# Optimization experiments

Hardware: AMD Instinct MI355X
Metric: run time of the kernel (lower is better)

The kernel has to match this reference:

```python
import jax, jax.numpy as jnp
import numpy as np

N_NODES = 40000
N_EDGES = 640000


def _sage_conv(x, src, dst, W_nb, b, W_self, n_nodes):
    # message = x[src] gathered per edge; mean-aggregate at dst (PyG SAGEConv, aggr='mean')
    msgs = x[src]  # [E, d]
    agg = jax.ops.segment_sum(msgs, dst, num_segments=n_nodes)  # [N, d]
    deg = jax.ops.segment_sum(jnp.ones((src.shape[0],), dtype=x.dtype), dst, num_segments=n_nodes)
    mean = agg / jnp.maximum(deg, 1.0)[:, None]
    # lin_l(aggregated) with bias + lin_r(self) without bias
    return mean @ W_nb + b + x @ W_self


def setup_inputs() -> dict:
    key = jax.random.key(0)
    ks = jax.random.split(key, 8)
    in_dim, h1, h2, out_dim = 128, 128, 64, 40
    s = lambda k, shp, d: jax.random.normal(k, shp, dtype=jnp.float32) / np.sqrt(d)
    return {
        "x": jax.random.normal(ks[0], (N_NODES, in_dim), dtype=jnp.float32),
        "edge_index": jax.random.randint(ks[1], (2, N_EDGES), 0, N_NODES, dtype=jnp.int64) if jax.config.jax_enable_x64 else jax.random.randint(ks[1], (2, N_EDGES), 0, N_NODES).astype(jnp.int32),
        "W1_nb": s(ks[2], (in_dim, h1), in_dim),
        "b1": jnp.zeros((h1,), dtype=jnp.float32),
        "W1_self": s(ks[3], (in_dim, h1), in_dim),
        "W2_nb": s(ks[4], (h1, h2), h1),
        "b2": jnp.zeros((h2,), dtype=jnp.float32),
        "W2_self": s(ks[5], (h1, h2), h1),
        "Wfc": s(ks[6], (h2, out_dim), h2),
        "bfc": jnp.zeros((out_dim,), dtype=jnp.float32),
    }


def reference(x, edge_index, W1_nb, b1, W1_self, W2_nb, b2, W2_self, Wfc, bfc):
    src, dst = edge_index[0], edge_index[1]
    h = jax.nn.relu(_sage_conv(x, src, dst, W1_nb, b1, W1_self, N_NODES))
    h = jax.nn.relu(_sage_conv(h, src, dst, W2_nb, b2, W2_self, N_NODES))
    embedding = h
    logits = h @ Wfc + bfc
    return (embedding, logits)
```

## Files before the change

### kernel.cpp

```cpp
#include <hip/hip_runtime.h>
#include <hip/hip_bf16.h>


#define N_NODES 40000
#define N_EDGES 640000
#define D_IN    128
#define D_H1    128
#define D_H2    64
#define D_OUT   40

#define SCAN_BLK 1024
#define N_SCAN_BLKS ((N_NODES + SCAN_BLK - 1) / SCAN_BLK)

typedef __attribute__((ext_vector_type(8))) short short8v;
typedef __attribute__((ext_vector_type(4))) float float4v;

__device__ __forceinline__ unsigned short f2bf(float f) {
    unsigned u = __float_as_uint(f);
    unsigned r = u + 0x7FFFu + ((u >> 16) & 1u);
    return (unsigned short)(r >> 16);
}
__device__ __forceinline__ float bf2f(unsigned short b) {
    return __uint_as_float(((unsigned)b) << 16);
}


__global__ void hist_k(const int* __restrict__ dst, int* __restrict__ deg) {
    int e = blockIdx.x * blockDim.x + threadIdx.x;
    if (e < N_EDGES) atomicAdd(&deg[dst[e]], 1);
}

__global__ __launch_bounds__(SCAN_BLK) void scan1_k(const int* __restrict__ deg,
                                                    int* __restrict__ blocksum) {
    __shared__ int wsum[SCAN_BLK / 64];
    int t = threadIdx.x;
    int i = blockIdx.x * SCAN_BLK + t;
    int v = (i < N_NODES) ? deg[i] : 0;
    #pragma unroll
    for (int s = 32; s > 0; s >>= 1) v += __shfl_down(v, s);
    if ((t & 63) == 0) wsum[t >> 6] = v;
    __syncthreads();
    if (t < SCAN_BLK / 64) {
        int x = wsum[t];
        #pragma unroll
        for (int s = SCAN_BLK / 128; s > 0; s >>= 1) x += __shfl_down(x, s);
        if (t == 0) blocksum[blockIdx.x] = x;
    }
}

__global__ __launch_bounds__(SCAN_BLK) void scan3_k(const int* __restrict__ deg,
                                                    const int* __restrict__ blocksum,
                                                    int* __restrict__ offsets,
                                                    int* __restrict__ cursor) {
    __shared__ int sm[SCAN_BLK];
    __shared__ int base_s;
    int t = threadIdx.x;
    int i = blockIdx.x * SCAN_BLK + t;
    if (t == 0) {
        int b = 0;
        for (int j = 0; j < (int)blockIdx.x; j++) b += blocksum[j];
        base_s = b;
        if (blockIdx.x == N_SCAN_BLKS - 1)
            offsets[N_NODES] = b + blocksum[blockIdx.x];
    }
    int v = (i < N_NODES) ? deg[i] : 0;
    sm[t] = v;
    __syncthreads();
    for (int s = 1; s < SCAN_BLK; s <<= 1) {
        int u = (t >= s) ? sm[t - s] : 0;
        __syncthreads();
        sm[t] += u;
        __syncthreads();
    }
    if (i < N_NODES) {
        int excl = base_s + sm[t] - v;
        offsets[i] = excl;
        cursor[i] = excl;
    }
}

__global__ void place_k(const int* __restrict__ src, const int* __restrict__ dst,
                        int* __restrict__ cursor, int* __restrict__ src_sorted) {
    int e = blockIdx.x * blockDim.x + threadIdx.x;
    if (e < N_EDGES) {
        int p = atomicAdd(&cursor[dst[e]], 1);
        src_sorted[p] = src[e];
    }
}


template <int D, int STRIDE>
__global__ __launch_bounds__(256) void agg_k(const float* __restrict__ feat,
                                             const int* __restrict__ offsets,
                                             const int* __restrict__ srcs,
                                             float* __restrict__ mean_out) {
    constexpr int LPN = D / 4;
    constexpr int NPB = 256 / LPN;
    int t = threadIdx.x;
    int g = t / LPN;
    int q = t % LPN;
    int node = blockIdx.x * NPB + g;
    int beg = offsets[node];
    int end = offsets[node + 1];
    float4 accA = {0.f, 0.f, 0.f, 0.f}, accB = {0.f, 0.f, 0.f, 0.f};
    int i = beg;
    for (; i + 8 <= end; i += 8) {
        float4 v[8];
        #pragma unroll
        for (int j = 0; j < 8; j++) {
            int s = srcs[i + j];
            v[j] = *(const float4*)(feat + (size_t)s * STRIDE + q * 4);
        }
        #pragma unroll
        for (int j = 0; j < 4; j++) {
            accA.x += v[j].x; accA.y += v[j].y; accA.z += v[j].z; accA.w += v[j].w;
            accB.x += v[j+4].x; accB.y += v[j+4].y; accB.z += v[j+4].z; accB.w += v[j+4].w;
        }
    }
    for (; i < end; ++i) {
        float4 v = *(const float4*)(feat + (size_t)srcs[i] * STRIDE + q * 4);
        accA.x += v.x; accA.y += v.y; accA.z += v.z; accA.w += v.w;
    }
    int cnt = end - beg;
    float inv = 1.0f / (float)(cnt > 1 ? cnt : 1);
    float4 r;
    r.x = (accA.x + accB.x) * inv; r.y = (accA.y + accB.y) * inv;
    r.z = (accA.z + accB.z) * inv; r.w = (accA.w + accB.w) * inv;
    *(float4*)(mean_out + (size_t)node * D + q * 4) = r;
}


__device__ __forceinline__ void wsplit_one(const float* W, int K, int N, int tid,
                                           short* Wt_hi, short* Wt_lo) {
    int k = tid / N, n = tid - k * N;
    float w = W[tid];
    unsigned short h = f2bf(w);
    unsigned short lo = f2bf(w - bf2f(h));
    Wt_hi[n * K + k] = (short)h;
    Wt_lo[n * K + k] = (short)lo;
}

__global__ void wsplit_all_k(const float* __restrict__ W1nb, const float* __restrict__ W1sf,
                             const float* __restrict__ W2nb, const float* __restrict__ W2sf,
                             short* __restrict__ o1nbh, short* __restrict__ o1nbl,
                             short* __restrict__ o1sfh, short* __restrict__ o1sfl,
                             short* __restrict__ o2nbh, short* __restrict__ o2nbl,
                             short* __restrict__ o2sfh, short* __restrict__ o2sfl) {
    int tid = blockIdx.x * blockDim.x + threadIdx.x;
    if (tid < 16384)      wsplit_one(W1nb, 128, 128, tid,          o1nbh, o1nbl);
    else if (tid < 32768) wsplit_one(W1sf, 128, 128, tid - 16384,  o1sfh, o1sfl);
    else if (tid < 40960) wsplit_one(W2nb, 128, 64,  tid - 32768,  o2nbh, o2nbl);
    else if (tid < 49152) wsplit_one(W2sf, 128, 64,  tid - 40960,  o2sfh, o2sfl);
}


template <int NOUT>
__global__ __launch_bounds__(256) void sage_mfma_k(
    const float* __restrict__ A1, const float* __restrict__ A2,
    const short* __restrict__ W1h, const short* __restrict__ W1l,
    const short* __restrict__ W2h, const short* __restrict__ W2l,
    const float* __restrict__ bias, float* __restrict__ out) {
    __shared__ short wh_s[64 * 128];
    __shared__ short wl_s[64 * 128];

    const int t = threadIdx.x;
    const int w = t >> 6;
    const int l = t & 63;
    const int ln16 = l & 15;
    const int kgrp = l >> 4;
    const int arow = blockIdx.x * 32 + (w & 1) * 16 + ln16;
    const int colbase = blockIdx.y * 64;
    const int cw = (w >> 1) * 32;

    float4v acc[2];
    #pragma unroll
    for (int ct = 0; ct < 2; ct++) {
        float bv = bias[colbase + cw + ct * 16 + ln16];
        acc[ct] = (float4v){bv, bv, bv, bv};
    }

    for (int phase = 0; phase < 2; ++phase) {
        const float* __restrict__ A  = phase ? A2 : A1;
        const short* __restrict__ Wh = phase ? W2h : W1h;
        const short* __restrict__ Wl = phase ? W2l : W1l;

        __syncthreads();

        float4 a0[4], a1[4];
        const float* ap = A + (size_t)arow * 128 + kgrp * 8;
        #pragma unroll
        for (int kc = 0; kc < 4; kc++) {
            a0[kc] = *(const float4*)(ap + kc * 32);
            a1[kc] = *(const float4*)(ap + kc * 32 + 4);
        }

        #pragma unroll
        for (int it = 0; it < 4; it++) {
            int fid = t + it * 256;
            int r = fid >> 4, c = fid & 15;
            int gofs = (colbase + r) * 128 + c * 8;
            int byte = (r * 256 + c * 16) ^ ((r & 7) << 4);
            *(int4*)((char*)wh_s + byte) = *(const int4*)(Wh + gofs);
            *(int4*)((char*)wl_s + byte) = *(const int4*)(Wl + gofs);
        }

        short8v ah[4], al[4];
        #pragma unroll
        for (int kc = 0; kc < 4; kc++) {
            #pragma unroll
            for (int j = 0; j < 4; j++) {
                float f0 = (&a0[kc].x)[j];
                float f1 = (&a1[kc].x)[j];
                unsigned short h0 = f2bf(f0), h1 = f2bf(f1);
                ah[kc][j]     = (short)h0;
                ah[kc][j + 4] = (short)h1;
                al[kc][j]     = (short)f2bf(f0 - bf2f(h0));
                al[kc][j + 4] = (short)f2bf(f1 - bf2f(h1));
            }
        }

        __syncthreads();

        #pragma unroll
        for (int kc = 0; kc < 4; kc++) {
            #pragma unroll
            for (int ct = 0; ct < 2; ct++) {
                int col = cw + ct * 16 + ln16;
                int byte = (col * 256 + kc * 64 + kgrp * 16) ^ ((col & 7) << 4);
                short8v bh = *(const short8v*)((const char*)wh_s + byte);
                short8v bl = *(const short8v*)((const char*)wl_s + byte);
                acc[ct] = __builtin_amdgcn_mfma_f32_16x16x32_bf16(ah[kc], bh, acc[ct], 0, 0, 0);
                acc[ct] = __builtin_amdgcn_mfma_f32_16x16x32_bf16(ah[kc], bl, acc[ct], 0, 0, 0);
                acc[ct] = __builtin_amdgcn_mfma_f32_16x16x32_bf16(al[kc], bh, acc[ct], 0, 0, 0);
            }
        }
    }

    #pragma unroll
    for (int ct = 0; ct < 2; ct++) {
        #pragma unroll
        for (int r = 0; r < 4; r++) {
            int row = blockIdx.x * 32 + (w & 1) * 16 + kgrp * 4 + r;
            int col = colbase + cw + ct * 16 + ln16;
            out[(size_t)row * NOUT + col] = fmaxf(acc[ct][r], 0.f);
        }
    }
}


__global__ __launch_bounds__(256) void gemm2_k(
    const float* __restrict__ A,
    const short* __restrict__ Wnbh, const short* __restrict__ Wnbl,
    const short* __restrict__ Wsfh, const short* __restrict__ Wsfl,
    const float* __restrict__ b2, float* __restrict__ zs2) {
    __shared__ short wh_s[64 * 128];
    __shared__ short wl_s[64 * 128];

    const int t = threadIdx.x;
    const int w = t >> 6;
    const int l = t & 63;
    const int ln16 = l & 15;
    const int kgrp = l >> 4;
    const int arow = blockIdx.x * 32 + (w & 1) * 16 + ln16;
    const int ysel = blockIdx.y;
    const int cw = (w >> 1) * 32;

    const short* __restrict__ Wh = ysel ? Wsfh : Wnbh;
    const short* __restrict__ Wl = ysel ? Wsfl : Wnbl;

    float4v acc[2];
    #pragma unroll
    for (int ct = 0; ct < 2; ct++) {
        float bv = ysel ? b2[cw + ct * 16 + ln16] : 0.f;
        acc[ct] = (float4v){bv, bv, bv, bv};
    }

    float4 a0[4], a1[4];
    const float* ap = A + (size_t)arow * 128 + kgrp * 8;
    #pragma unroll
    for (int kc = 0; kc < 4; kc++) {
        a0[kc] = *(const float4*)(ap + kc * 32);
        a1[kc] = *(const float4*)(ap + kc * 32 + 4);
    }

    #pragma unroll
    for (int it = 0; it < 4; it++) {
        int fid = t + it * 256;
        int r = fid >> 4, c = fid & 15;
        int gofs = r * 128 + c * 8;
        int byte = (r * 256 + c * 16) ^ ((r & 7) << 4);
        *(int4*)((char*)wh_s + byte) = *(const int4*)(Wh + gofs);
        *(int4*)((char*)wl_s + byte) = *(const int4*)(Wl + gofs);
    }

    short8v ah[4], al[4];
    #pragma unroll
    for (int kc = 0; kc < 4; kc++) {
        #pragma unroll
        for (int j = 0; j < 4; j++) {
            float f0 = (&a0[kc].x)[j];
            float f1 = (&a1[kc].x)[j];
            unsigned short h0 = f2bf(f0), h1 = f2bf(f1);
            ah[kc][j]     = (short)h0;
            ah[kc][j + 4] = (short)h1;
            al[kc][j]     = (short)f2bf(f0 - bf2f(h0));
            al[kc][j + 4] = (short)f2bf(f1 - bf2f(h1));
        }
    }

    __syncthreads();

    #pragma unroll
    for (int kc = 0; kc < 4; kc++) {
        #pragma unroll
        for (int ct = 0; ct < 2; ct++) {
            int col = cw + ct * 16 + ln16;
            int byte = (col * 256 + kc * 64 + kgrp * 16) ^ ((col & 7) << 4);
            short8v bh = *(const short8v*)((const char*)wh_s + byte);
            short8v bl = *(const short8v*)((const char*)wl_s + byte);
            acc[ct] = __builtin_amdgcn_mfma_f32_16x16x32_bf16(ah[kc], bh, acc[ct], 0, 0, 0);
            acc[ct] = __builtin_amdgcn_mfma_f32_16x16x32_bf16(ah[kc], bl, acc[ct], 0, 0, 0);
            acc[ct] = __builtin_amdgcn_mfma_f32_16x16x32_bf16(al[kc], bh, acc[ct], 0, 0, 0);
        }
    }

    #pragma unroll
    for (int ct = 0; ct < 2; ct++) {
        #pragma unroll
        for (int r = 0; r < 4; r++) {
            int row = blockIdx.x * 32 + (w & 1) * 16 + kgrp * 4 + r;
            int col = ysel * 64 + cw + ct * 16 + ln16;
            zs2[(size_t)row * 128 + col] = acc[ct][r];
        }
    }
}


__global__ __launch_bounds__(256) void final_k(const float* __restrict__ mean2,
                                               const float* __restrict__ zs2,
                                               const float* __restrict__ Wfc,
                                               const float* __restrict__ bfc,
                                               float* __restrict__ emb,
                                               float* __restrict__ logits) {
    __shared__ float es[16][68];
    int t = threadIdx.x;
    int g = t >> 4;
    int q = t & 15;
    int node = blockIdx.x * 16 + g;
    float4 m = *(const float4*)(mean2 + (size_t)node * 64 + q * 4);
    float4 s = *(const float4*)(zs2 + (size_t)node * 128 + 64 + q * 4);
    float4 e;
    e.x = fmaxf(m.x + s.x, 0.f);
    e.y = fmaxf(m.y + s.y, 0.f);
    e.z = fmaxf(m.z + s.z, 0.f);
    e.w = fmaxf(m.w + s.w, 0.f);
    *(float4*)(emb + (size_t)node * 64 + q * 4) = e;
    *(float4*)&es[g][q * 4] = e;
    __syncthreads();
    #pragma unroll
    for (int j = 0; j < 3; j++) {
        int c = q + 16 * j;
        if (c < D_OUT) {
            float acc = bfc[c];
            #pragma unroll
            for (int k = 0; k < 64; k++) acc += es[g][k] * Wfc[k * D_OUT + c];
            logits[(size_t)node * D_OUT + c] = acc;
        }
    }
}


extern "C" void kernel_launch(void* const* d_in, const int* in_sizes, int n_in,
                              void* d_out, int out_size, void* d_ws, size_t ws_size,
                              hipStream_t stream) {
    const float* x       = (const float*)d_in[0];
    const int*   ei      = (const int*)d_in[1];
    const float* W1_nb   = (const float*)d_in[2];
    const float* b1      = (const float*)d_in[3];
    const float* W1_self = (const float*)d_in[4];
    const float* W2_nb   = (const float*)d_in[5];
    const float* b2      = (const float*)d_in[6];
    const float* W2_self = (const float*)d_in[7];
    const float* Wfc     = (const float*)d_in[8];
    const float* bfc     = (const float*)d_in[9];

    const int* src = ei;
    const int* dst = ei + N_EDGES;

    char* w = (char*)d_ws;
    int* deg        = (int*)w;
    int* offsets    = deg + N_NODES;
    int* cursor     = offsets + (N_NODES + 1);
    int* blocksum   = cursor + N_NODES;
    int* src_sorted = blocksum + N_SCAN_BLKS;
    size_t int_elems = (size_t)N_NODES * 3 + 1 + N_SCAN_BLKS + N_EDGES;
    size_t int_bytes = (int_elems * 4 + 15) & ~(size_t)15;
    float* bufA = (float*)(w + int_bytes);
    float* bufB = bufA + (size_t)N_NODES * 128;
    short* w1nb_h   = (short*)(bufB + (size_t)N_NODES * 128);
    short* w1nb_l   = w1nb_h + 128 * 128;
    short* w1self_h = w1nb_l + 128 * 128;
    short* w1self_l = w1self_h + 128 * 128;
    short* w2nb_h   = w1self_l + 128 * 128;
    short* w2nb_l   = w2nb_h + 128 * 64;
    short* w2self_h = w2nb_l + 128 * 64;
    short* w2self_l = w2self_h + 128 * 64;

    float* emb    = (float*)d_out;
    float* logits = emb + (size_t)N_NODES * D_H2;

    wsplit_all_k<<<(49152 + 255) / 256, 256, 0, stream>>>(
        W1_nb, W1_self, W2_nb, W2_self,
        w1nb_h, w1nb_l, w1self_h, w1self_l, w2nb_h, w2nb_l, w2self_h, w2self_l);

    hipMemsetAsync(deg, 0, N_NODES * sizeof(int), stream);
    hist_k<<<(N_EDGES + 255) / 256, 256, 0, stream>>>(dst, deg);
    scan1_k<<<N_SCAN_BLKS, SCAN_BLK, 0, stream>>>(deg, blocksum);
    scan3_k<<<N_SCAN_BLKS, SCAN_BLK, 0, stream>>>(deg, blocksum, offsets, cursor);
    place_k<<<(N_EDGES + 255) / 256, 256, 0, stream>>>(src, dst, cursor, src_sorted);

    agg_k<128, 128><<<N_NODES / 8, 256, 0, stream>>>(x, offsets, src_sorted, bufA);
    sage_mfma_k<128><<<dim3(N_NODES / 32, 2), 256, 0, stream>>>(
        bufA, x, w1nb_h, w1nb_l, w1self_h, w1self_l, b1, bufB);

    gemm2_k<<<dim3(N_NODES / 32, 2), 256, 0, stream>>>(
        bufB, w2nb_h, w2nb_l, w2self_h, w2self_l, b2, bufA);

    agg_k<64, 128><<<N_NODES / 16, 256, 0, stream>>>(bufA, offsets, src_sorted, bufB);

    final_k<<<N_NODES / 16, 256, 0, stream>>>(bufB, bufA, Wfc, bfc, emb, logits);
}
```

Before: 294.0 us.

## Gather neighbor features in fp16 and fuse layer-2 aggregation with final projection

Converts x to fp16 up front so the layer-1 neighbor gather moves half the bytes per edge. The layer-2 neighbor projection is also written as fp16 into a compact 64-wide buffer. The second aggregation is fused with the bias/ReLU/logits kernel, which removes one launch and one intermediate round trip. Storing the gathered features in fp16 adds rounding error compared with the fp32 gathers and may loosen accuracy. An extra conversion pass over x is added.

After: 264.1 us. 1.11x faster.

```diff
diff --git a/kernel.cpp b/kernel.cpp
--- a/kernel.cpp
+++ b/kernel.cpp
@@ -1,5 +1,6 @@
 #include <hip/hip_runtime.h>
 #include <hip/hip_bf16.h>
+#include <hip/hip_fp16.h>
 
 
 #define N_NODES 40000
@@ -13,6 +14,7 @@
 #define N_SCAN_BLKS ((N_NODES + SCAN_BLK - 1) / SCAN_BLK)
 
 typedef __attribute__((ext_vector_type(8))) short short8v;
+typedef __attribute__((ext_vector_type(8))) _Float16 half8v;
 typedef __attribute__((ext_vector_type(4))) float float4v;
 
 __device__ __forceinline__ unsigned short f2bf(float f) {
@@ -89,12 +91,24 @@
 }
 
 
-template <int D, int STRIDE>
-__global__ __launch_bounds__(256) void agg_k(const float* __restrict__ feat,
-                                             const int* __restrict__ offsets,
-                                             const int* __restrict__ srcs,
-                                             float* __restrict__ mean_out) {
-    constexpr int LPN = D / 4;
+__global__ void xh_k(const float* __restrict__ x, _Float16* __restrict__ xh) {
+    int i = blockIdx.x * blockDim.x + threadIdx.x;
+    if (i >= N_NODES * D_IN / 8) return;
+    float4 a = ((const float4*)x)[i * 2];
+    float4 b = ((const float4*)x)[i * 2 + 1];
+    half8v h;
+    h[0] = (_Float16)a.x; h[1] = (_Float16)a.y; h[2] = (_Float16)a.z; h[3] = (_Float16)a.w;
+    h[4] = (_Float16)b.x; h[5] = (_Float16)b.y; h[6] = (_Float16)b.z; h[7] = (_Float16)b.w;
+    ((half8v*)xh)[i] = h;
+}
+
+
+template <int D>
+__global__ __launch_bounds__(256) void aggh_k(const _Float16* __restrict__ feat,
+                                              const int* __restrict__ offsets,
+                                              const int* __restrict__ srcs,
+                                              float* __restrict__ mean_out) {
+    constexpr int LPN = D / 8;
     constexpr int NPB = 256 / LPN;
     int t = threadIdx.x;
     int g = t / LPN;
@@ -102,31 +116,31 @@
     int node = blockIdx.x * NPB + g;
     int beg = offsets[node];
     int end = offsets[node + 1];
-    float4 accA = {0.f, 0.f, 0.f, 0.f}, accB = {0.f, 0.f, 0.f, 0.f};
+    float acc[8] = {0.f, 0.f, 0.f, 0.f, 0.f, 0.f, 0.f, 0.f};
     int i = beg;
     for (; i + 8 <= end; i += 8) {
-        float4 v[8];
+        half8v v[8];
+        #pragma unroll
+        for (int j = 0; j < 8; j++)
+            v[j] = *(const half8v*)(feat + (size_t)srcs[i + j] * D + q * 8);
         #pragma unroll
         for (int j = 0; j < 8; j++) {
-            int s = srcs[i + j];
-            v[j] = *(const float4*)(feat + (size_t)s * STRIDE + q * 4);
-        }
-        #pragma unroll
-        for (int j = 0; j < 4; j++) {
-            accA.x += v[j].x; accA.y += v[j].y; accA.z += v[j].z; accA.w += v[j].w;
-            accB.x += v[j+4].x; accB.y += v[j+4].y; accB.z += v[j+4].z; accB.w += v[j+4].w;
+            #pragma unroll
+            for (int k = 0; k < 8; k++) acc[k] += (float)v[j][k];
         }
     }
     for (; i < end; ++i) {
-        float4 v = *(const float4*)(feat + (size_t)srcs[i] * STRIDE + q * 4);
-        accA.x += v.x; accA.y += v.y; accA.z += v.z; accA.w += v.w;
+        half8v v = *(const half8v*)(feat + (size_t)srcs[i] * D + q * 8);
+        #pragma unroll
+        for (int k = 0; k < 8; k++) acc[k] += (float)v[k];
     }
     int cnt = end - beg;
     float inv = 1.0f / (float)(cnt > 1 ? cnt : 1);
-    float4 r;
-    r.x = (accA.x + accB.x) * inv; r.y = (accA.y + accB.y) * inv;
-    r.z = (accA.z + accB.z) * inv; r.w = (accA.w + accB.w) * inv;
-    *(float4*)(mean_out + (size_t)node * D + q * 4) = r;
+    float4 r0, r1;
+    r0.x = acc[0] * inv; r0.y = acc[1] * inv; r0.z = acc[2] * inv; r0.w = acc[3] * inv;
+    r1.x = acc[4] * inv; r1.y = acc[5] * inv; r1.z = acc[6] * inv; r1.w = acc[7] * inv;
+    *(float4*)(mean_out + (size_t)node * D + q * 8) = r0;
+    *(float4*)(mean_out + (size_t)node * D + q * 8 + 4) = r1;
 }
 
 
@@ -252,7 +266,8 @@
     const float* __restrict__ A,
     const short* __restrict__ Wnbh, const short* __restrict__ Wnbl,
     const short* __restrict__ Wsfh, const short* __restrict__ Wsfl,
-    const float* __restrict__ b2, float* __restrict__ zs2) {
+    const float* __restrict__ b2,
+    _Float16* __restrict__ z2nb, float* __restrict__ zself) {
     __shared__ short wh_s[64 * 128];
     __shared__ short wl_s[64 * 128];
 
@@ -329,43 +344,77 @@
         #pragma unroll
         for (int r = 0; r < 4; r++) {
             int row = blockIdx.x * 32 + (w & 1) * 16 + kgrp * 4 + r;
-            int col = ysel * 64 + cw + ct * 16 + ln16;
-            zs2[(size_t)row * 128 + col] = acc[ct][r];
-        }
-    }
-}
-
-
-__global__ __launch_bounds__(256) void final_k(const float* __restrict__ mean2,
-                                               const float* __restrict__ zs2,
-                                               const float* __restrict__ Wfc,
-                                               const float* __restrict__ bfc,
-                                               float* __restrict__ emb,
-                                               float* __restrict__ logits) {
-    __shared__ float es[16][68];
+            int col = cw + ct * 16 + ln16;
+            if (ysel == 0) z2nb[(size_t)row * 64 + col] = (_Float16)acc[ct][r];
+            else           zself[(size_t)row * 64 + col] = acc[ct][r];
+        }
+    }
+}
+
+
+__global__ __launch_bounds__(256) void agg2final_k(const _Float16* __restrict__ z2nb,
+                                                   const float* __restrict__ zself,
+                                                   const int* __restrict__ offsets,
+                                                   const int* __restrict__ srcs,
+                                                   const float* __restrict__ Wfc,
+                                                   const float* __restrict__ bfc,
+                                                   float* __restrict__ emb,
+                                                   float* __restrict__ logits) {
+    __shared__ float es[32][68];
     int t = threadIdx.x;
-    int g = t >> 4;
-    int q = t & 15;
-    int node = blockIdx.x * 16 + g;
-    float4 m = *(const float4*)(mean2 + (size_t)node * 64 + q * 4);
-    float4 s = *(const float4*)(zs2 + (size_t)node * 128 + 64 + q * 4);
-    float4 e;
-    e.x = fmaxf(m.x + s.x, 0.f);
-    e.y = fmaxf(m.y + s.y, 0.f);
-    e.z = fmaxf(m.z + s.z, 0.f);
-    e.w = fmaxf(m.w + s.w, 0.f);
-    *(float4*)(emb + (size_t)node * 64 + q * 4) = e;
-    *(float4*)&es[g][q * 4] = e;
+    int g = t >> 3;
+    int q = t & 7;
+    int node = blockIdx.x * 32 + g;
+    int beg = offsets[node];
+    int end = offsets[node + 1];
+    float acc[8] = {0.f, 0.f, 0.f, 0.f, 0.f, 0.f, 0.f, 0.f};
+    int i = beg;
+    for (; i + 8 <= end; i += 8) {
+        half8v v[8];
+        #pragma unroll
+        for (int j = 0; j < 8; j++)
+            v[j] = *(const half8v*)(z2nb + (size_t)srcs[i + j] * 64 + q * 8);
+        #pragma unroll
+        for (int j = 0; j < 8; j++) {
+            #pragma unroll
+            for (int k = 0; k < 8; k++) acc[k] += (float)v[j][k];
+        }
+    }
+    for (; i < end; ++i) {
+        half8v v = *(const half8v*)(z2nb + (size_t)srcs[i] * 64 + q * 8);
+        #pragma unroll
+        for (int k = 0; k < 8; k++) acc[k] += (float)v[k];
+    }
+    int cnt = end - beg;
+    float inv = 1.0f / (float)(cnt > 1 ? cnt : 1);
+    float4 s0 = *(const float4*)(zself + (size_t)node * 64 + q * 8);
+    float4 s1 = *(const float4*)(zself + (size_t)node * 64 + q * 8 + 4);
+    float e[8];
+    e[0] = fmaxf(acc[0] * inv + s0.x, 0.f);
+    e[1] = fmaxf(acc[1] * inv + s0.y, 0.f);
+    e[2] = fmaxf(acc[2] * inv + s0.z, 0.f);
+    e[3] = fmaxf(acc[3] * inv + s0.w, 0.f);
+    e[4] = fmaxf(acc[4] * inv + s1.x, 0.f);
+    e[5] = fmaxf(acc[5] * inv + s1.y, 0.f);
+    e[6] = fmaxf(acc[6] * inv + s1.z, 0.f);
+    e[7] = fmaxf(acc[7] * inv + s1.w, 0.f);
+    float4 o0 = {e[0], e[1], e[2], e[3]};
+    float4 o1 = {e[4], e[5], e[6], e[7]};
+    *(float4*)(emb + (size_t)node * 64 + q * 8) = o0;
+    *(float4*)(emb + (size_t)node * 64 + q * 8 + 4) = o1;
+    #pragma unroll
+    for (int k = 0; k < 8; k++) es[g][q * 8 + k] = e[k];
     __syncthreads();
     #pragma unroll
-    for (int j = 0; j < 3; j++) {
-        int c = q + 16 * j;
-        if (c < D_OUT) {
-            float acc = bfc[c];
-            #pragma unroll
-            for (int k = 0; k < 64; k++) acc += es[g][k] * Wfc[k * D_OUT + c];
-            logits[(size_t)node * D_OUT + c] = acc;
-        }
+    for (int j = 0; j < 5; j++) {
+        int o = t + 256 * j;
+        int ng = o / D_OUT;
+        int c = o - ng * D_OUT;
+        int gnode = blockIdx.x * 32 + ng;
+        float a = bfc[c];
+        #pragma unroll
+        for (int k = 0; k < 64; k++) a += es[ng][k] * Wfc[k * D_OUT + c];
+        logits[(size_t)gnode * D_OUT + c] = a;
     }
 }
 
@@ -395,9 +444,12 @@
     int* src_sorted = blocksum + N_SCAN_BLKS;
     size_t int_elems = (size_t)N_NODES * 3 + 1 + N_SCAN_BLKS + N_EDGES;
     size_t int_bytes = (int_elems * 4 + 15) & ~(size_t)15;
-    float* bufA = (float*)(w + int_bytes);
-    float* bufB = bufA + (size_t)N_NODES * 128;
-    short* w1nb_h   = (short*)(bufB + (size_t)N_NODES * 128);
+    float* mean1 = (float*)(w + int_bytes);
+    _Float16* z2nb = (_Float16*)mean1;
+    float* zself = (float*)((char*)mean1 + (size_t)N_NODES * 64 * sizeof(_Float16));
+    float* h1    = mean1 + (size_t)N_NODES * 128;
+    _Float16* xh = (_Float16*)h1;
+    short* w1nb_h   = (short*)(h1 + (size_t)N_NODES * 128);
     short* w1nb_l   = w1nb_h + 128 * 128;
     short* w1self_h = w1nb_l + 128 * 128;
     short* w1self_l = w1self_h + 128 * 128;
@@ -412,6 +464,7 @@
     wsplit_all_k<<<(49152 + 255) / 256, 256, 0, stream>>>(
         W1_nb, W1_self, W2_nb, W2_self,
         w1nb_h, w1nb_l, w1self_h, w1self_l, w2nb_h, w2nb_l, w2self_h, w2self_l);
+    xh_k<<<(N_NODES * D_IN / 8 + 255) / 256, 256, 0, stream>>>(x, xh);
 
     hipMemsetAsync(deg, 0, N_NODES * sizeof(int), stream);
     hist_k<<<(N_EDGES + 255) / 256, 256, 0, stream>>>(dst, deg);
@@ -419,14 +472,13 @@
     scan3_k<<<N_SCAN_BLKS, SCAN_BLK, 0, stream>>>(deg, blocksum, offsets, cursor);
     place_k<<<(N_EDGES + 255) / 256, 256, 0, stream>>>(src, dst, cursor, src_sorted);
 
-    agg_k<128, 128><<<N_NODES / 8, 256, 0, stream>>>(x, offsets, src_sorted, bufA);
+    aggh_k<128><<<N_NODES / 16, 256, 0, stream>>>(xh, offsets, src_sorted, mean1);
     sage_mfma_k<128><<<dim3(N_NODES / 32, 2), 256, 0, stream>>>(
-        bufA, x, w1nb_h, w1nb_l, w1self_h, w1self_l, b1, bufB);
+        mean1, x, w1nb_h, w1nb_l, w1self_h, w1self_l, b1, h1);
 
     gemm2_k<<<dim3(N_NODES / 32, 2), 256, 0, stream>>>(
-        bufB, w2nb_h, w2nb_l, w2self_h, w2self_l, b2, bufA);
-
-    agg_k<64, 128><<<N_NODES / 16, 256, 0, stream>>>(bufA, offsets, src_sorted, bufB);
-
-    final_k<<<N_NODES / 16, 256, 0, stream>>>(bufB, bufA, Wfc, bfc, emb, logits);
-}
+        h1, w2nb_h, w2nb_l, w2self_h, w2self_l, b2, z2nb, zself);
+
+    agg2final_k<<<N_NODES / 32, 256, 0, stream>>>(
+        z2nb, zself, offsets, src_sorted, Wfc, bfc, emb, logits);
+}
```
